# Performance work log

Measured on AMD Instinct MI355X. Metric: run time of the kernel, lower is better.

The kernel has to match this reference:

```python
import jax, jax.numpy as jnp
import numpy as np

B, D, L, H = 8, 512, 2048, 8
DH = D // H
NEG = -1e30


def setup_inputs() -> dict:
    key = jax.random.key(0)
    k1, k2, k3, k4 = jax.random.split(key, 4)
    queries = jax.random.normal(k1, (B, D, L), dtype=jnp.float32)
    mask = jax.random.randint(k2, (B, L), 0, 2, dtype=jnp.int32)
    w_mem = jax.random.normal(k3, (2 * D, D), dtype=jnp.float32) * (1.0 / np.sqrt(D))
    w_q = jax.random.normal(k4, (D, D), dtype=jnp.float32) * (1.0 / np.sqrt(D))
    return {"queries": queries, "mask": mask, "w_mem": w_mem, "w_q": w_q}


def reference(queries, mask, w_mem, w_q):
    # 1x1 conv == pointwise GEMM over channel dim. queries: [B, D, L]
    memory = jnp.einsum('od,bdl->blo', w_mem, queries)  # [B, L, 2D]
    query = jnp.einsum('od,bdl->blo', w_q, queries)     # [B, L, D]

    def split_heads(x):  # [B, L, C] -> [B, H, L, C/H]
        b, l, c = x.shape
        return x.reshape(b, l, H, c // H).transpose(0, 2, 1, 3)

    k, v = memory[..., :D], memory[..., D:]
    Q = split_heads(query) * (DH ** -0.5)  # [B, H, L, DH]
    K = split_heads(k)
    V = split_heads(v)

    logits = jnp.einsum('bhqd,bhkd->bhqk', Q, K)  # [B, H, L, L]
    m = mask.astype(jnp.float32)[:, None, None, :]  # [B, 1, 1, L]
    logits = logits * m + (1.0 - m) * NEG
    weights = jax.nn.softmax(logits, axis=-1)
    x = jnp.einsum('bhqk,bhkd->bhqd', weights, V)  # [B, H, L, DH]
    # combine heads -> [B, L, D] -> transpose back to [B, D, L]
    out = x.transpose(0, 2, 1, 3).reshape(B, L, D).transpose(0, 2, 1)
    return out
```

## Files before the change

kernel.cpp:

```cpp
#include <hip/hip_runtime.h>
#include <hip/hip_bf16.h>

#define NB 8
#define ND 512
#define NL 2048
#define NH 8
#define NDH 64
#define VROWS 72

typedef __attribute__((ext_vector_type(8))) short bf16x8;
typedef __attribute__((ext_vector_type(4))) float f32x4;
typedef __attribute__((ext_vector_type(4))) unsigned int u32x4;

__device__ __forceinline__ unsigned short f2bf(float x) {
    return (unsigned short)((__float_as_uint(x) + 0x8000u) >> 16);
}

__device__ __forceinline__ float exp2_fast(float x) {
#if __has_builtin(__builtin_amdgcn_exp2f)
    return __builtin_amdgcn_exp2f(x);
#else
    return exp2f(x);
#endif
}

__device__ __forceinline__ unsigned int pack_bf16(float a, float b) {
#if __has_builtin(__builtin_amdgcn_cvt_pk_bf16_f32)
    auto r = __builtin_amdgcn_cvt_pk_bf16_f32(a, b);
    unsigned int u;
    __builtin_memcpy(&u, &r, 4);
    return u;
#else
    unsigned int ua = __float_as_uint(a) + 0x8000u;
    unsigned int ub = __float_as_uint(b) + 0x8000u;
    return __builtin_amdgcn_perm(ub, ua, 0x07060302u);
#endif
}

__device__ __forceinline__ int perm64(int k) {
    return (k & 32) | ((k & 12) << 1) | ((k & 16) >> 2) | (k & 3);
}

__device__ __forceinline__ void async16(void* lds, const void* g) {
    __builtin_amdgcn_global_load_lds(
        (const __attribute__((address_space(1))) unsigned int*)g,
        (__attribute__((address_space(3))) unsigned int*)lds, 16, 0, 0);
}

__global__ __launch_bounds__(256) void prep(
    const float* __restrict__ qin,
    const float* __restrict__ w_mem, const float* __restrict__ w_q,
    const int* __restrict__ maskp,
    unsigned short* __restrict__ Xt, unsigned short* __restrict__ Wc,
    unsigned short* __restrict__ Vt, unsigned short* __restrict__ Kh,
    int* __restrict__ ilist, int* __restrict__ ntile, int* __restrict__ nvalid)
{
    const int bid = blockIdx.x;
    const int t = threadIdx.x;
    if (bid < 2048) {
        __shared__ __align__(16) unsigned short T[64][72];
        const int l0 = (bid & 31) * 64, d0 = ((bid >> 5) & 7) * 64, b = bid >> 8;
        const float* X = qin + ((size_t)b * ND + d0) * NL + l0;
        #pragma unroll
        for (int i = 0; i < 4; ++i) {
            int e = t + i * 256;
            int d = e >> 4, l4 = (e & 15) * 4;
            float4 v = *(const float4*)(X + (size_t)d * NL + l4);
            T[l4 + 0][d] = f2bf(v.x);
            T[l4 + 1][d] = f2bf(v.y);
            T[l4 + 2][d] = f2bf(v.z);
            T[l4 + 3][d] = f2bf(v.w);
        }
        __syncthreads();
        #pragma unroll
        for (int i = 0; i < 2; ++i) {
            int e = t + i * 256;
            int row = e >> 3, c8 = (e & 7) * 8;
            *(bf16x8*)(Xt + ((size_t)b * NL + l0 + row) * ND + d0 + c8) =
                *(const bf16x8*)&T[row][c8];
        }
    } else if (bid < 2432) {
        int idx = ((bid - 2048) * 256 + t) * 8;
        int o = idx >> 9, k = idx & 511;
        const float* src;
        float sc;
        if (o < 1024) { src = w_mem + (size_t)o * ND + k; sc = 1.0f; }
        else          { src = w_q + (size_t)(o - 1024) * ND + k;
                        sc = 0.125f * 1.4426950408889634f; }
        float4 f0 = *(const float4*)src;
        float4 f1 = *(const float4*)(src + 4);
        ushort4 p0 = { f2bf(f0.x * sc), f2bf(f0.y * sc), f2bf(f0.z * sc), f2bf(f0.w * sc) };
        ushort4 p1 = { f2bf(f1.x * sc), f2bf(f1.y * sc), f2bf(f1.z * sc), f2bf(f1.w * sc) };
        *(ushort4*)(Wc + idx) = p0;
        *(ushort4*)(Wc + idx + 4) = p1;
    } else {
        __shared__ int wsum[4];
        const int b = bid - 2432;
        const int lane = t & 63, wv = t >> 6;
        int4 ma = *(const int4*)&maskp[b * NL + t * 8];
        int4 mb = *(const int4*)&maskp[b * NL + t * 8 + 4];
        int m[8] = {ma.x, ma.y, ma.z, ma.w, mb.x, mb.y, mb.z, mb.w};
        int loc = 0;
        #pragma unroll
        for (int i = 0; i < 8; ++i) loc += m[i];
        int sc = loc;
        #pragma unroll
        for (int off = 1; off < 64; off <<= 1) {
            int v = __shfl_up(sc, off);
            if (lane >= off) sc += v;
        }
        if (lane == 63) wsum[wv] = sc;
        __syncthreads();
        int wbase = 0;
        #pragma unroll
        for (int i = 0; i < 4; ++i) if (i < wv) wbase += wsum[i];
        int j = wbase + sc - loc;
        #pragma unroll
        for (int i = 0; i < 8; ++i) {
            if (m[i]) ilist[b * NL + j] = t * 8 + i;
            j += m[i];
        }
        const int nb = wsum[0] + wsum[1] + wsum[2] + wsum[3];
        const int Nt = (nb + 63) & ~63;
        if (t == 0) { ntile[b] = Nt >> 6; nvalid[b] = nb; }
        const int Nt2 = (nb + 127) & ~127;
        for (int e = nb + t; e < Nt2; e += 256) ilist[b * NL + e] = 0;
        const int pad = Nt - nb;
        for (int h = 0; h < NH; ++h) {
            unsigned short* row64 = Vt + (((size_t)(b * NH + h)) * VROWS + 64) * NL;
            for (int jj = t; jj < Nt; jj += 256)
                row64[(jj & ~63) | perm64(jj & 63)] =
                    (jj < nb) ? (unsigned short)0x3F80 : (unsigned short)0;
            for (int e = t; e < pad * 64; e += 256) {
                int jj = nb + (e >> 6), dd = e & 63;
                int slot = (jj & ~63) | perm64(jj & 63);
                Vt[(((size_t)(b * NH + h)) * VROWS + dd) * NL + slot] = 0;
                Kh[(((size_t)(b * NH + h)) * NL + jj) * NDH + dd] = 0;
            }
        }
    }
}

__global__ __launch_bounds__(256, 3) void proj_mfma(
    const unsigned short* __restrict__ Wc,
    const unsigned short* __restrict__ Xt,
    const int* __restrict__ ilist,
    const int* __restrict__ ntilep,
    const int* __restrict__ nvalidp,
    unsigned short* __restrict__ Kh,
    unsigned short* __restrict__ Qh,
    unsigned short* __restrict__ Vt)
{
    __shared__ __align__(16) unsigned short As[128 * 64];
    __shared__ __align__(16) unsigned short Bs[128 * 64];

    const int b  = blockIdx.z;
    const int m0 = blockIdx.y * 128;
    const int n0 = blockIdx.x * 128;
    const int t  = threadIdx.x;
    const int w = t >> 6, lane = t & 63, quad = lane >> 4, lq = lane & 15;
    const int wo = (w >> 1) * 64, wl = (w & 1) * 64;
    const int lr = lane >> 3;
    const int cbsw = (lane & 7) ^ lr;
    const bool isQ = (m0 >= 1024);
    const bool isV = (m0 >= 512) && !isQ;
    const f32x4 z4 = {0.f, 0.f, 0.f, 0.f};
    const int sw[2] = {(quad ^ (lq & 7)) * 8, ((4 + quad) ^ (lq & 7)) * 8};

    int nb = NL;
    if (!isQ) {
        const int Nt = ntilep[b] * 64;
        if (n0 >= Nt) return;
        nb = nvalidp[b];
    }

    const unsigned short* bsrc[4];
    #pragma unroll
    for (int jx = 0; jx < 4; ++jx) {
        int row = n0 + w * 8 + 32 * jx + lr;
        int l = isQ ? row : ilist[b * NL + row];
        bsrc[jx] = Xt + ((size_t)b * NL + l) * ND + cbsw * 8;
    }

    f32x4 acc[4][4];
    #pragma unroll
    for (int im = 0; im < 4; ++im)
        #pragma unroll
        for (int in = 0; in < 4; ++in) acc[im][in] = z4;

    if (!isV) {
        for (int k0 = 0; k0 < ND; k0 += 64) {
            __syncthreads();
            #pragma unroll
            for (int jx = 0; jx < 4; ++jx) {
                int R = (w + 4 * jx) * 8;
                async16(&As[R * 64],
                        Wc + (size_t)(m0 + R + lr) * ND + k0 + cbsw * 8);
            }
            #pragma unroll
            for (int jx = 0; jx < 4; ++jx) {
                int R = (w + 4 * jx) * 8;
                async16(&Bs[R * 64], bsrc[jx] + k0);
            }
            __syncthreads();
            #pragma unroll
            for (int ks = 0; ks < 2; ++ks) {
                bf16x8 af[4], bfr[4];
                #pragma unroll
                for (int im = 0; im < 4; ++im)
                    af[im] = *(const bf16x8*)&As[(wo + im * 16 + lq) * 64 + sw[ks]];
                #pragma unroll
                for (int in = 0; in < 4; ++in)
                    bfr[in] = *(const bf16x8*)&Bs[(wl + in * 16 + lq) * 64 + sw[ks]];
                #pragma unroll
                for (int im = 0; im < 4; ++im)
                    #pragma unroll
                    for (int in = 0; in < 4; ++in)
                        acc[im][in] = __builtin_amdgcn_mfma_f32_16x16x32_bf16(
                            af[im], bfr[in], acc[im][in], 0, 0, 0);
            }
        }
        if (m0 < 512) {
            #pragma unroll
            for (int im = 0; im < 4; ++im) {
                int o  = (m0 + wo + im * 16 + quad * 4) & 511;
                int hh = o >> 6, dh = o & 63;
                #pragma unroll
                for (int in = 0; in < 4; ++in) {
                    int j = n0 + wl + in * 16 + lq;
                    if (j < nb) {
                        ushort4 pk = { f2bf(acc[im][in][0]), f2bf(acc[im][in][1]),
                                       f2bf(acc[im][in][2]), f2bf(acc[im][in][3]) };
                        *(ushort4*)&Kh[(((size_t)b * NH + hh) * NL + j) * NDH + dh] = pk;
                    }
                }
            }
        } else {
            #pragma unroll
            for (int im = 0; im < 4; ++im) {
                int o  = (m0 + wo + im * 16 + quad * 4) & 511;
                int hh = o >> 6, dh = o & 63;
                #pragma unroll
                for (int in = 0; in < 4; ++in) {
                    int l = n0 + wl + in * 16 + lq;
                    ushort4 pk = { f2bf(acc[im][in][0]), f2bf(acc[im][in][1]),
                                   f2bf(acc[im][in][2]), f2bf(acc[im][in][3]) };
                    *(ushort4*)&Qh[(((size_t)b * NH + hh) * NL + l) * NDH + dh] = pk;
                }
            }
        }
    } else {
        for (int k0 = 0; k0 < ND; k0 += 64) {
            __syncthreads();
            #pragma unroll
            for (int jx = 0; jx < 4; ++jx) {
                int R = (w + 4 * jx) * 8;
                async16(&As[R * 64],
                        Wc + (size_t)(m0 + R + lr) * ND + k0 + cbsw * 8);
            }
            #pragma unroll
            for (int jx = 0; jx < 4; ++jx) {
                int R = (w + 4 * jx) * 8;
                async16(&Bs[R * 64], bsrc[jx] + k0);
            }
            __syncthreads();
            #pragma unroll
            for (int ks = 0; ks < 2; ++ks) {
                bf16x8 af[4], bfr[4];
                #pragma unroll
                for (int im = 0; im < 4; ++im)
                    af[im] = *(const bf16x8*)&As[(wo + im * 16 + lq) * 64 + sw[ks]];
                #pragma unroll
                for (int in = 0; in < 4; ++in)
                    bfr[in] = *(const bf16x8*)&Bs[(wl + in * 16 + lq) * 64 + sw[ks]];
                #pragma unroll
                for (int im = 0; im < 4; ++im)
                    #pragma unroll
                    for (int in = 0; in < 4; ++in)
                        acc[im][in] = __builtin_amdgcn_mfma_f32_16x16x32_bf16(
                            bfr[im], af[in], acc[im][in], 0, 0, 0);
            }
        }
        #pragma unroll
        for (int im = 0; im < 4; ++im) {
            int j4 = n0 + wl + im * 16 + quad * 4;
            int slot[4];
            bool ok[4];
            #pragma unroll
            for (int r = 0; r < 4; ++r) {
                int j = j4 + r;
                ok[r] = (j < nb);
                slot[r] = (j & ~63) | perm64(j & 63);
            }
            #pragma unroll
            for (int in = 0; in < 4; ++in) {
                int o  = m0 - 512 + wo + in * 16 + lq;
                int hh = o >> 6, dd = o & 63;
                const size_t rowbase = (((size_t)(b * NH + hh)) * VROWS + dd) * NL;
                #pragma unroll
                for (int r = 0; r < 4; ++r)
                    if (ok[r])
                        Vt[rowbase + slot[r]] = f2bf(acc[im][in][r]);
            }
        }
    }
}

__global__ __launch_bounds__(512, 4) void attn_mfma(
    const unsigned short* __restrict__ Qh,
    const unsigned short* __restrict__ Kh,
    const unsigned short* __restrict__ Vt,
    const int* __restrict__ ntilep,
    float* __restrict__ out)
{
    __shared__ __align__(16) unsigned short Ks2[2][64 * 64];
    __shared__ __align__(16) unsigned short Vs2[2][80 * 64];

    const int id = blockIdx.x;
    const int h  = id & 7;
    const int b  = (id >> 3) & 7;
    const int q0 = (id >> 6) * 256;
    const int t = threadIdx.x;
    const int w = t >> 6;
    const int lane = t & 63, quad = lane >> 4, lq = lane & 15;
    const int lr = lane >> 3;
    const int cbsw = (lane & 7) ^ lr;
    const f32x4 z4 = {0.f, 0.f, 0.f, 0.f};

    const unsigned short* Qg = Qh + ((size_t)(b * NH + h)) * NL * NDH;
    const unsigned short* Kg = Kh + ((size_t)(b * NH + h)) * NL * NDH;
    const unsigned short* Vg = Vt + ((size_t)(b * NH + h)) * VROWS * NL;
    const int ntiles = ntilep[b];

    const int sw0 = (quad ^ (lq & 7)) * 8;
    const int sw1 = ((4 + quad) ^ (lq & 7)) * 8;

    const unsigned short* kgp = Kg + (size_t)(w * 8 + lr) * NDH + cbsw * 8;
    const unsigned short* vgp = Vg + (size_t)(w * 8 + lr) * NL + cbsw * 8;
    const unsigned short* vgm = Vg + (size_t)(64 + lr) * NL + cbsw * 8;

    auto stage = [&](unsigned short* Kd, unsigned short* Vd, int kn) {
        async16(Kd + w * 512, kgp + (size_t)kn * NDH);
        async16(Vd + w * 512, vgp + kn);
        if (w == 7) async16(Vd + 8 * 512, vgm + kn);
    };

    stage(Ks2[0], Vs2[0], 0);

    bf16x8 qf[2][2];
    #pragma unroll
    for (int ni = 0; ni < 2; ++ni)
        #pragma unroll
        for (int ks = 0; ks < 2; ++ks)
            qf[ni][ks] = *(const bf16x8*)
                &Qg[(size_t)(q0 + w * 32 + ni * 16 + lq) * NDH + ks * 32 + quad * 8];

    f32x4 oacc[5][2];
    #pragma unroll
    for (int dm = 0; dm < 5; ++dm)
        #pragma unroll
        for (int ni = 0; ni < 2; ++ni) oacc[dm][ni] = z4;

    auto body = [&](const unsigned short* KsB, const unsigned short* VsB,
                    unsigned short* KsN, unsigned short* VsN,
                    int kn, bool pf) {
        __syncthreads();
        if (pf) stage(KsN, VsN, kn);

        const unsigned short* kb0 = KsB + lq * 64 + sw0;
        const unsigned short* kb1 = KsB + lq * 64 + sw1;
        const unsigned short* vb0 = VsB + lq * 64 + sw0;
        const unsigned short* vb1 = VsB + lq * 64 + sw1;

        f32x4 sacc[4][2];
        #pragma unroll
        for (int mi = 0; mi < 4; ++mi) {
            bf16x8 kf = *(const bf16x8*)&kb0[mi * 1024];
            sacc[mi][0] = __builtin_amdgcn_mfma_f32_16x16x32_bf16(kf, qf[0][0], z4, 0, 0, 0);
            sacc[mi][1] = __builtin_amdgcn_mfma_f32_16x16x32_bf16(kf, qf[1][0], z4, 0, 0, 0);
        }
        #pragma unroll
        for (int mi = 0; mi < 4; ++mi) {
            bf16x8 kf = *(const bf16x8*)&kb1[mi * 1024];
            sacc[mi][0] = __builtin_amdgcn_mfma_f32_16x16x32_bf16(kf, qf[0][1], sacc[mi][0], 0, 0, 0);
            sacc[mi][1] = __builtin_amdgcn_mfma_f32_16x16x32_bf16(kf, qf[1][1], sacc[mi][1], 0, 0, 0);
        }

        #pragma unroll
        for (int ks = 0; ks < 2; ++ks) {
            u32x4 pfu[2];
            #pragma unroll
            for (int half = 0; half < 2; ++half) {
                const int mi = ks * 2 + half, jp = half * 2;
                #pragma unroll
                for (int ni = 0; ni < 2; ++ni) {
                    float e0 = exp2_fast(sacc[mi][ni][0]);
                    float e1 = exp2_fast(sacc[mi][ni][1]);
                    float e2 = exp2_fast(sacc[mi][ni][2]);
                    float e3 = exp2_fast(sacc[mi][ni][3]);
                    pfu[ni][jp + 0] = pack_bf16(e0, e1);
                    pfu[ni][jp + 1] = pack_bf16(e2, e3);
                }
            }
            const unsigned short* vb = ks ? vb1 : vb0;
            #pragma unroll
            for (int dm = 0; dm < 5; ++dm) {
                bf16x8 vf = *(const bf16x8*)&vb[dm * 1024];
                oacc[dm][0] = __builtin_amdgcn_mfma_f32_16x16x32_bf16(
                    vf, __builtin_bit_cast(bf16x8, pfu[0]), oacc[dm][0], 0, 0, 0);
                oacc[dm][1] = __builtin_amdgcn_mfma_f32_16x16x32_bf16(
                    vf, __builtin_bit_cast(bf16x8, pfu[1]), oacc[dm][1], 0, 0, 0);
            }
        }
    };

    int kt = 0;
    #pragma unroll 1
    for (; kt + 2 <= ntiles; kt += 2) {
        body(Ks2[0], Vs2[0], Ks2[1], Vs2[1], (kt + 1) * 64, true);
        body(Ks2[1], Vs2[1], Ks2[0], Vs2[0], (kt + 2) * 64, kt + 2 < ntiles);
    }
    if (kt < ntiles)
        body(Ks2[0], Vs2[0], Ks2[1], Vs2[1], 0, false);

    float inv[2];
    #pragma unroll
    for (int ni = 0; ni < 2; ++ni)
        inv[ni] = 1.0f / __shfl(oacc[4][ni][0], lq);

    #pragma unroll
    for (int dm = 0; dm < 4; ++dm)
        #pragma unroll
        for (int ni = 0; ni < 2; ++ni)
            #pragma unroll
            for (int r = 0; r < 4; ++r) {
                int dh = dm * 16 + quad * 4 + r;
                int l  = q0 + w * 32 + ni * 16 + lq;
                out[((size_t)b * ND + h * NDH + dh) * NL + l] =
                    oacc[dm][ni][r] * inv[ni];
            }
}

extern "C" void kernel_launch(void* const* d_in, const int* in_sizes, int n_in,
                              void* d_out, int out_size, void* d_ws, size_t ws_size,
                              hipStream_t stream) {
    const float* queries = (const float*)d_in[0];
    const int*   maskp   = (const int*)d_in[1];
    const float* w_mem   = (const float*)d_in[2];
    const float* w_q     = (const float*)d_in[3];
    float* out = (float*)d_out;

    const size_t headElems  = (size_t)NB * NH * NL * NDH;
    const size_t vElems     = (size_t)NB * NH * VROWS * NL;
    unsigned short* Kh = (unsigned short*)d_ws;
    unsigned short* Vt = Kh + headElems;
    unsigned short* Qh = Vt + vElems;
    unsigned short* Wc = Qh + headElems;
    unsigned short* Xt = Wc + (size_t)1536 * ND;
    int* ilist  = (int*)(Xt + (size_t)NB * NL * ND);
    int* ntile  = ilist + NB * NL;
    int* nvalid = ntile + NB;

    prep<<<2440, 256, 0, stream>>>(queries, w_mem, w_q, maskp,
                                   Xt, Wc, Vt, Kh, ilist, ntile, nvalid);

    dim3 g1(NL / 128, 1536 / 128, NB);
    proj_mfma<<<g1, 256, 0, stream>>>(Wc, Xt, ilist, ntile, nvalid, Kh, Qh, Vt);

    attn_mfma<<<512, 512, 0, stream>>>(Qh, Kh, Vt, ntile, out);
}
```

Baseline: 184.4 us.

## Store transposed activations in mask-compacted order to drop gather in projection

The prep transpose blocks now each compute the mask prefix sum and write Xt rows in a permuted order: valid positions first, masked ones after. The projection kernel can then load its B tiles contiguously instead of gathering through an index list. Q outputs are scattered back to their original positions through the stored permutation. This adds a redundant per-block mask scan in prep and a scattered Q store in exchange for contiguous loads in the GEMM. The load loop is also restructured so each wave issues A and B tile loads with a single interleaved index.

```diff
diff --git a/kernel.cpp b/kernel.cpp
--- a/kernel.cpp
+++ b/kernel.cpp
@@ -53,30 +53,69 @@
     const int* __restrict__ maskp,
     unsigned short* __restrict__ Xt, unsigned short* __restrict__ Wc,
     unsigned short* __restrict__ Vt, unsigned short* __restrict__ Kh,
-    int* __restrict__ ilist, int* __restrict__ ntile, int* __restrict__ nvalid)
+    int* __restrict__ fperm, int* __restrict__ ntile, int* __restrict__ nvalid)
 {
     const int bid = blockIdx.x;
     const int t = threadIdx.x;
     if (bid < 2048) {
         __shared__ __align__(16) unsigned short T[64][72];
+        __shared__ int dstsh[64];
+        __shared__ int wsumX[4];
         const int l0 = (bid & 31) * 64, d0 = ((bid >> 5) & 7) * 64, b = bid >> 8;
+        const int lane = t & 63, wv = t >> 6;
+
+        int4 ma = *(const int4*)&maskp[b * NL + t * 8];
+        int4 mb = *(const int4*)&maskp[b * NL + t * 8 + 4];
+        int m[8] = {ma.x, ma.y, ma.z, ma.w, mb.x, mb.y, mb.z, mb.w};
+        int loc = 0;
+        #pragma unroll
+        for (int i = 0; i < 8; ++i) loc += m[i];
+        int sc = loc;
+        #pragma unroll
+        for (int off = 1; off < 64; off <<= 1) {
+            int v = __shfl_up(sc, off);
+            if (lane >= off) sc += v;
+        }
+        if (lane == 63) wsumX[wv] = sc;
+
         const float* X = qin + ((size_t)b * ND + d0) * NL + l0;
+        float4 vv[4];
         #pragma unroll
         for (int i = 0; i < 4; ++i) {
             int e = t + i * 256;
             int d = e >> 4, l4 = (e & 15) * 4;
-            float4 v = *(const float4*)(X + (size_t)d * NL + l4);
-            T[l4 + 0][d] = f2bf(v.x);
-            T[l4 + 1][d] = f2bf(v.y);
-            T[l4 + 2][d] = f2bf(v.z);
-            T[l4 + 3][d] = f2bf(v.w);
+            vv[i] = *(const float4*)(X + (size_t)d * NL + l4);
+        }
+        __syncthreads();
+        int wbase = 0;
+        #pragma unroll
+        for (int i = 0; i < 4; ++i) if (i < wv) wbase += wsumX[i];
+        const int nb = wsumX[0] + wsumX[1] + wsumX[2] + wsumX[3];
+        if ((t >> 3) == (l0 >> 6)) {
+            int base = t * 8 - l0;
+            int p = wbase + sc - loc;
+            #pragma unroll
+            for (int i = 0; i < 8; ++i) {
+                int l = t * 8 + i;
+                dstsh[base + i] = m[i] ? p : nb + (l - p);
+                p += m[i];
+            }
+        }
+        #pragma unroll
+        for (int i = 0; i < 4; ++i) {
+            int e = t + i * 256;
+            int d = e >> 4, l4 = (e & 15) * 4;
+            T[l4 + 0][d] = f2bf(vv[i].x);
+            T[l4 + 1][d] = f2bf(vv[i].y);
+            T[l4 + 2][d] = f2bf(vv[i].z);
+            T[l4 + 3][d] = f2bf(vv[i].w);
         }
         __syncthreads();
         #pragma unroll
         for (int i = 0; i < 2; ++i) {
             int e = t + i * 256;
             int row = e >> 3, c8 = (e & 7) * 8;
-            *(bf16x8*)(Xt + ((size_t)b * NL + l0 + row) * ND + d0 + c8) =
+            *(bf16x8*)(Xt + ((size_t)b * NL + dstsh[row]) * ND + d0 + c8) =
                 *(const bf16x8*)&T[row][c8];
         }
     } else if (bid < 2432) {
@@ -114,28 +153,27 @@
         int wbase = 0;
         #pragma unroll
         for (int i = 0; i < 4; ++i) if (i < wv) wbase += wsum[i];
-        int j = wbase + sc - loc;
+        const int nb = wsum[0] + wsum[1] + wsum[2] + wsum[3];
+        int jj = wbase + sc - loc;
         #pragma unroll
         for (int i = 0; i < 8; ++i) {
-            if (m[i]) ilist[b * NL + j] = t * 8 + i;
-            j += m[i];
-        }
-        const int nb = wsum[0] + wsum[1] + wsum[2] + wsum[3];
+            int l = t * 8 + i;
+            fperm[b * NL + (m[i] ? jj : nb + (l - jj))] = l;
+            jj += m[i];
+        }
         const int Nt = (nb + 63) & ~63;
         if (t == 0) { ntile[b] = Nt >> 6; nvalid[b] = nb; }
-        const int Nt2 = (nb + 127) & ~127;
-        for (int e = nb + t; e < Nt2; e += 256) ilist[b * NL + e] = 0;
         const int pad = Nt - nb;
         for (int h = 0; h < NH; ++h) {
             unsigned short* row64 = Vt + (((size_t)(b * NH + h)) * VROWS + 64) * NL;
-            for (int jj = t; jj < Nt; jj += 256)
-                row64[(jj & ~63) | perm64(jj & 63)] =
-                    (jj < nb) ? (unsigned short)0x3F80 : (unsigned short)0;
+            for (int j2 = t; j2 < Nt; j2 += 256)
+                row64[(j2 & ~63) | perm64(j2 & 63)] =
+                    (j2 < nb) ? (unsigned short)0x3F80 : (unsigned short)0;
             for (int e = t; e < pad * 64; e += 256) {
-                int jj = nb + (e >> 6), dd = e & 63;
-                int slot = (jj & ~63) | perm64(jj & 63);
+                int j2 = nb + (e >> 6), dd = e & 63;
+                int slot = (j2 & ~63) | perm64(j2 & 63);
                 Vt[(((size_t)(b * NH + h)) * VROWS + dd) * NL + slot] = 0;
-                Kh[(((size_t)(b * NH + h)) * NL + jj) * NDH + dd] = 0;
+                Kh[(((size_t)(b * NH + h)) * NL + j2) * NDH + dd] = 0;
             }
         }
     }
@@ -144,7 +182,7 @@
 __global__ __launch_bounds__(256, 3) void proj_mfma(
     const unsigned short* __restrict__ Wc,
     const unsigned short* __restrict__ Xt,
-    const int* __restrict__ ilist,
+    const int* __restrict__ fperm,
     const int* __restrict__ ntilep,
     const int* __restrict__ nvalidp,
     unsigned short* __restrict__ Kh,
@@ -169,17 +207,8 @@
 
     int nb = NL;
     if (!isQ) {
-        const int Nt = ntilep[b] * 64;
-        if (n0 >= Nt) return;
+        if (n0 >= ntilep[b] * 64) return;
         nb = nvalidp[b];
-    }
-
-    const unsigned short* bsrc[4];
-    #pragma unroll
-    for (int jx = 0; jx < 4; ++jx) {
-        int row = n0 + w * 8 + 32 * jx + lr;
-        int l = isQ ? row : ilist[b * NL + row];
-        bsrc[jx] = Xt + ((size_t)b * NL + l) * ND + cbsw * 8;
     }
 
     f32x4 acc[4][4];
@@ -189,18 +218,25 @@
         for (int in = 0; in < 4; ++in) acc[im][in] = z4;
 
     if (!isV) {
+        int lor[4];
+        if (isQ) {
+            #pragma unroll
+            for (int in = 0; in < 4; ++in)
+                lor[in] = fperm[b * NL + n0 + wl + in * 16 + lq];
+        }
         for (int k0 = 0; k0 < ND; k0 += 64) {
             __syncthreads();
-            #pragma unroll
-            for (int jx = 0; jx < 4; ++jx) {
-                int R = (w + 4 * jx) * 8;
-                async16(&As[R * 64],
-                        Wc + (size_t)(m0 + R + lr) * ND + k0 + cbsw * 8);
-            }
-            #pragma unroll
-            for (int jx = 0; jx < 4; ++jx) {
-                int R = (w + 4 * jx) * 8;
-                async16(&Bs[R * 64], bsrc[jx] + k0);
+            #pragma unroll 2
+            for (int i = w; i < 32; i += 4) {
+                if (i < 16) {
+                    int R = i * 8;
+                    async16(&As[R * 64],
+                            Wc + (size_t)(m0 + R + lr) * ND + k0 + cbsw * 8);
+                } else {
+                    int R = (i - 16) * 8;
+                    async16(&Bs[R * 64],
+                            Xt + ((size_t)b * NL + n0 + R + lr) * ND + k0 + cbsw * 8);
+                }
             }
             __syncthreads();
             #pragma unroll
@@ -242,26 +278,26 @@
                 int hh = o >> 6, dh = o & 63;
                 #pragma unroll
                 for (int in = 0; in < 4; ++in) {
-                    int l = n0 + wl + in * 16 + lq;
                     ushort4 pk = { f2bf(acc[im][in][0]), f2bf(acc[im][in][1]),
                                    f2bf(acc[im][in][2]), f2bf(acc[im][in][3]) };
-                    *(ushort4*)&Qh[(((size_t)b * NH + hh) * NL + l) * NDH + dh] = pk;
+                    *(ushort4*)&Qh[(((size_t)b * NH + hh) * NL + lor[in]) * NDH + dh] = pk;
                 }
             }
         }
     } else {
         for (int k0 = 0; k0 < ND; k0 += 64) {
             __syncthreads();
-            #pragma unroll
-            for (int jx = 0; jx < 4; ++jx) {
-                int R = (w + 4 * jx) * 8;
-                async16(&As[R * 64],
-                        Wc + (size_t)(m0 + R + lr) * ND + k0 + cbsw * 8);
-            }
-            #pragma unroll
-            for (int jx = 0; jx < 4; ++jx) {
-                int R = (w + 4 * jx) * 8;
-                async16(&Bs[R * 64], bsrc[jx] + k0);
+            #pragma unroll 2
+            for (int i = w; i < 32; i += 4) {
+                if (i < 16) {
+                    int R = i * 8;
+                    async16(&As[R * 64],
+                            Wc + (size_t)(m0 + R + lr) * ND + k0 + cbsw * 8);
+                } else {
+                    int R = (i - 16) * 8;
+                    async16(&Bs[R * 64],
+                            Xt + ((size_t)b * NL + n0 + R + lr) * ND + k0 + cbsw * 8);
+                }
             }
             __syncthreads();
             #pragma unroll
@@ -457,15 +493,15 @@
     unsigned short* Qh = Vt + vElems;
     unsigned short* Wc = Qh + headElems;
     unsigned short* Xt = Wc + (size_t)1536 * ND;
-    int* ilist  = (int*)(Xt + (size_t)NB * NL * ND);
-    int* ntile  = ilist + NB * NL;
+    int* fperm  = (int*)(Xt + (size_t)NB * NL * ND);
+    int* ntile  = fperm + NB * NL;
     int* nvalid = ntile + NB;
 
     prep<<<2440, 256, 0, stream>>>(queries, w_mem, w_q, maskp,
-                                   Xt, Wc, Vt, Kh, ilist, ntile, nvalid);
+                                   Xt, Wc, Vt, Kh, fperm, ntile, nvalid);
 
     dim3 g1(NL / 128, 1536 / 128, NB);
-    proj_mfma<<<g1, 256, 0, stream>>>(Wc, Xt, ilist, ntile, nvalid, Kh, Qh, Vt);
+    proj_mfma<<<g1, 256, 0, stream>>>(Wc, Xt, fperm, ntile, nvalid, Kh, Qh, Vt);
 
     attn_mfma<<<512, 512, 0, stream>>>(Qh, Kh, Vt, ntile, out);
 }
```

After: 191.0 us. +3.6%, slower.
